# Kernel optimization log

Measured on AMD Instinct MI355X. Metric: run time of the kernel, lower is better.

The kernel has to match this reference:

```python
import jax, jax.numpy as jnp
import numpy as np
from jax import lax

B, T, P, H, O = 64, 96, 256, 128, 24  # batch, seq_len, num_points, hidden_dim, pred_len


def setup_inputs() -> dict:
    key = jax.random.key(0)
    ks = jax.random.split(key, 7)
    s = 1.0 / np.sqrt(H)  # torch LSTM/Linear default init scale
    return {
        "x": jax.random.normal(ks[0], (B, T, P, 1), dtype=jnp.float32),
        "W_ih": jax.random.uniform(ks[1], (P, 4 * H, 1), jnp.float32, -s, s),
        "W_hh": jax.random.uniform(ks[2], (P, 4 * H, H), jnp.float32, -s, s),
        "b_ih": jax.random.uniform(ks[3], (P, 4 * H), jnp.float32, -s, s),
        "b_hh": jax.random.uniform(ks[4], (P, 4 * H), jnp.float32, -s, s),
        "W_fc": jax.random.uniform(ks[5], (P, O, H), jnp.float32, -s, s),
        "b_fc": jax.random.uniform(ks[6], (P, O), jnp.float32, -s, s),
    }


def reference(x, W_ih, W_hh, b_ih, b_hh, W_fc, b_fc):
    # x: [B, T, P, F]; model uses only feature 0
    xs = x[..., 0]  # [B, T, P]
    # input_dim == 1, so input-to-gate contribution is a scaled broadcast of W_ih
    # precompute for all timesteps: [T, B, P, 4H]
    gx = jnp.einsum("btp,pg->tbpg", xs, W_ih[:, :, 0]) + (b_ih + b_hh)

    def step(carry, gxt):
        h, c = carry  # [B, P, H] each
        gates = gxt + jnp.einsum("bph,pgh->bpg", h, W_hh)  # [B, P, 4H]
        i, f, g, o = jnp.split(gates, 4, axis=-1)  # torch gate order i,f,g,o
        i = jax.nn.sigmoid(i)
        f = jax.nn.sigmoid(f)
        g = jnp.tanh(g)
        o = jax.nn.sigmoid(o)
        c = f * c + i * g
        h = o * jnp.tanh(c)
        return (h, c), None

    h0 = jnp.zeros((B, P, H), dtype=x.dtype)
    (h, _), _ = lax.scan(step, (h0, h0), gx)
    # per-point Linear on final hidden state: [B, P, O]
    out = jnp.einsum("bph,poh->bpo", h, W_fc) + b_fc
    # original stacks point outputs on last dim -> [B, pred_len, P]
    return jnp.transpose(out, (0, 2, 1))
```

## Files before the change

kernel.cpp:

```cpp
#include <hip/hip_runtime.h>
#include <hip/hip_bf16.h>

#define Bdim 64
#define Tdim 96
#define Pdim 256
#define Hdim 128
#define Gdim 512
#define Odim 24
#define BH   32
#define WROW 132

typedef _Float16 f16x8 __attribute__((ext_vector_type(8)));
typedef float    f32x16 __attribute__((ext_vector_type(16)));

union H8 { uint2 u2[2]; unsigned short s[8]; _Float16 h[8]; f16x8 v; };
union HS { _Float16 h; unsigned short s; };

__device__ __forceinline__ float exp2_fast(float x) {
#if __has_builtin(__builtin_amdgcn_exp2f)
    return __builtin_amdgcn_exp2f(x);
#else
    return __expf(x * 0.6931471805599453f);
#endif
}

__global__ __launch_bounds__(1024, 4)
void lstm_fused(const float* __restrict__ x,
                const float* __restrict__ W_ih,
                const float* __restrict__ W_hh,
                const float* __restrict__ b_ih,
                const float* __restrict__ b_hh,
                const float* __restrict__ W_fc,
                const float* __restrict__ b_fc,
                float* __restrict__ out)
{
    __shared__ unsigned short hs[2][2][BH * WROW];

    const int p   = blockIdx.x;
    const int tid = threadIdx.x;
    const int w   = tid >> 6;
    const int l31 = tid & 31;
    const int hi  = (tid >> 5) & 1;

    const float L1 = 1.4426950408889634f;
    const float L2 = 2.0f * L1;

    for (int i = tid; i < 2 * 2 * BH * WROW; i += 1024) ((unsigned short*)hs)[i] = 0;

    f16x8 afr[9];
    {
        const int rp   = w * 32 + l31;
        const int orow = ((rp & 3) << 7) | (rp >> 2);
        const float sc = ((rp & 3) == 2) ? L2 : L1;
        const float* rowp = W_hh + (size_t)p * Gdim * Hdim + (size_t)orow * Hdim;
        #pragma unroll
        for (int ks = 0; ks < 8; ++ks) {
            int k0 = ks * 16 + hi * 8;
            float4 va = *(const float4*)(rowp + k0);
            float4 vb = *(const float4*)(rowp + k0 + 4);
            H8 u;
            u.h[0] = (_Float16)(sc * va.x); u.h[1] = (_Float16)(sc * va.y);
            u.h[2] = (_Float16)(sc * va.z); u.h[3] = (_Float16)(sc * va.w);
            u.h[4] = (_Float16)(sc * vb.x); u.h[5] = (_Float16)(sc * vb.y);
            u.h[6] = (_Float16)(sc * vb.z); u.h[7] = (_Float16)(sc * vb.w);
            afr[ks] = u.v;
        }
        H8 u9;
        #pragma unroll
        for (int j = 0; j < 8; ++j) u9.s[j] = 0;
        if (hi == 0) {
            u9.h[0] = (_Float16)(sc * W_ih[(size_t)p * Gdim + orow]);
            u9.h[1] = (_Float16)(sc * (b_ih[(size_t)p * Gdim + orow] +
                                       b_hh[(size_t)p * Gdim + orow]));
        }
        afr[8] = u9.v;
    }

    auto do_gemm = [&](const unsigned short* hb, float xv) -> f32x16 {
        f32x16 a;
        #pragma unroll
        for (int j = 0; j < 16; ++j) a[j] = 0.f;
        const char* hbase = (const char*)hb;
        #pragma unroll
        for (int ks = 0; ks < 8; ++ks) {
            int boff = l31 * (WROW * 2) + ks * 32 + hi * 16;
            H8 bb;
            bb.u2[0] = *(const uint2*)(hbase + boff);
            bb.u2[1] = *(const uint2*)(hbase + boff + 8);
            a = __builtin_amdgcn_mfma_f32_32x32x16_f16(afr[ks], bb.v, a, 0, 0, 0);
        }
        H8 bg;
        #pragma unroll
        for (int j = 0; j < 8; ++j) bg.s[j] = 0;
        if (hi == 0) { bg.h[0] = (_Float16)xv; bg.h[1] = (_Float16)1.0f; }
        a = __builtin_amdgcn_mfma_f32_32x32x16_f16(afr[8], bg.v, a, 0, 0, 0);
        return a;
    };

    auto do_ep = [&](const f32x16& a, float* cr, unsigned short* hw) {
        #pragma unroll
        for (int q = 0; q < 4; ++q) {
            float yi = a[4 * q + 0];
            float yf = a[4 * q + 1];
            float yg = a[4 * q + 2];
            float yo = a[4 * q + 3];
            float Ef = exp2_fast(-yf);
            float Ei = exp2_fast(-yi);
            float Eg = exp2_fast(yg);
            float t1 = 1.0f + Ef;
            float t2 = 1.0f + Ei;
            float t3 = Eg + 1.0f;
            float t4 = Eg - 1.0f;
            float den = (t1 * t2) * t3;
            float num = __builtin_fmaf(cr[q] * t2, t3, (L2 * t4) * t1);
            float cn  = num * __builtin_amdgcn_rcpf(den);
            cn = fminf(60.0f, fmaxf(-60.0f, cn));
            cr[q] = cn;
            float Eo = exp2_fast(-yo);
            float Ec = exp2_fast(cn);
            float hv = (Ec - 1.0f) * __builtin_amdgcn_rcpf((1.0f + Eo) * (Ec + 1.0f));
            HS s2; s2.h = (_Float16)hv;
            hw[l31 * WROW + (w * 8 + 2 * q + hi)] = s2.s;
        }
    };

    float cre0[4] = {0.f, 0.f, 0.f, 0.f};
    float cre1[4] = {0.f, 0.f, 0.f, 0.f};

    const float* xp0 = x + (size_t)((0 * BH + l31) * Tdim) * Pdim + p;
    const float* xp1 = x + (size_t)((1 * BH + l31) * Tdim) * Pdim + p;
    float xv0 = xp0[0];
    float xv1 = xp1[0];

    __syncthreads();

    int b0 = 0, b1 = 0;
    f32x16 acc0 = do_gemm(hs[0][b0], xv0);
    xv0 = xp0[(size_t)1 * Pdim];

    f32x16 acc1;
    for (int t = 0; t < Tdim; ++t) {
        acc1 = do_gemm(hs[1][b1], xv1);
        do_ep(acc0, cre0, hs[0][b0 ^ 1]);
        __syncthreads();
        b0 ^= 1;
        xv1 = (t + 1 < Tdim) ? xp1[(size_t)(t + 1) * Pdim] : 0.f;

        acc0 = do_gemm(hs[0][b0], xv0);
        do_ep(acc1, cre1, hs[1][b1 ^ 1]);
        __syncthreads();
        b1 ^= 1;
        xv0 = (t + 2 < Tdim) ? xp0[(size_t)(t + 2) * Pdim] : 0.f;
    }

    const float* wfc = W_fc + (size_t)p * Odim * Hdim;
    const float* bfc = b_fc + (size_t)p * Odim;
    for (int i = tid; i < Bdim * Odim; i += 1024) {
        int o = i % Odim;
        int b = i / Odim;
        const unsigned short* hr = (b < BH) ? (hs[0][b0] + b * WROW)
                                            : (hs[1][b1] + (b - BH) * WROW);
        float s = bfc[o];
        const float* wr = wfc + o * Hdim;
        #pragma unroll 8
        for (int k2 = 0; k2 < Hdim; ++k2) {
            HS s2; s2.s = hr[k2];
            s = __builtin_fmaf(wr[k2], (float)s2.h, s);
        }
        out[(size_t)b * Odim * Pdim + (size_t)o * Pdim + p] = s;
    }
}

extern "C" void kernel_launch(void* const* d_in, const int* in_sizes, int n_in,
                              void* d_out, int out_size, void* d_ws, size_t ws_size,
                              hipStream_t stream) {
    const float* x    = (const float*)d_in[0];
    const float* W_ih = (const float*)d_in[1];
    const float* W_hh = (const float*)d_in[2];
    const float* b_ih = (const float*)d_in[3];
    const float* b_hh = (const float*)d_in[4];
    const float* W_fc = (const float*)d_in[5];
    const float* b_fc = (const float*)d_in[6];
    float* out = (float*)d_out;

    lstm_fused<<<dim3(Pdim), dim3(1024), 0, stream>>>(x, W_ih, W_hh, b_ih, b_hh, W_fc, b_fc, out);
}
```

Measured before the change: 400.4 us.

## Merge batch-half pipeline into single step with one barrier and paired reciprocals

Replaces the staggered two-half schedule (GEMM of one half overlapped with epilogue of the other, two barriers per timestep) with a single step that runs both halves' MFMA chains interleaved, then a joint epilogue and one barrier. Reciprocals in the gate epilogue are shared between the two halves via a product trick, halving rcp count. This removes a barrier per timestep but gives up the cross-half overlap of matrix and transcendental work; the clamp on the cell value is tightened, which also limits overflow in the shared-reciprocal products.

```diff
diff --git a/kernel.cpp b/kernel.cpp
--- a/kernel.cpp
+++ b/kernel.cpp
@@ -12,6 +12,7 @@
 
 typedef _Float16 f16x8 __attribute__((ext_vector_type(8)));
 typedef float    f32x16 __attribute__((ext_vector_type(16)));
+typedef float    f32x2  __attribute__((ext_vector_type(2)));
 
 union H8 { uint2 u2[2]; unsigned short s[8]; _Float16 h[8]; f16x8 v; };
 union HS { _Float16 h; unsigned short s; };
@@ -76,81 +77,101 @@
         afr[8] = u9.v;
     }
 
-    auto do_gemm = [&](const unsigned short* hb, float xv) -> f32x16 {
-        f32x16 a;
-        #pragma unroll
-        for (int j = 0; j < 16; ++j) a[j] = 0.f;
-        const char* hbase = (const char*)hb;
-        #pragma unroll
-        for (int ks = 0; ks < 8; ++ks) {
-            int boff = l31 * (WROW * 2) + ks * 32 + hi * 16;
-            H8 bb;
-            bb.u2[0] = *(const uint2*)(hbase + boff);
-            bb.u2[1] = *(const uint2*)(hbase + boff + 8);
-            a = __builtin_amdgcn_mfma_f32_32x32x16_f16(afr[ks], bb.v, a, 0, 0, 0);
-        }
-        H8 bg;
-        #pragma unroll
-        for (int j = 0; j < 8; ++j) bg.s[j] = 0;
-        if (hi == 0) { bg.h[0] = (_Float16)xv; bg.h[1] = (_Float16)1.0f; }
-        a = __builtin_amdgcn_mfma_f32_32x32x16_f16(afr[8], bg.v, a, 0, 0, 0);
-        return a;
-    };
-
-    auto do_ep = [&](const f32x16& a, float* cr, unsigned short* hw) {
-        #pragma unroll
-        for (int q = 0; q < 4; ++q) {
-            float yi = a[4 * q + 0];
-            float yf = a[4 * q + 1];
-            float yg = a[4 * q + 2];
-            float yo = a[4 * q + 3];
-            float Ef = exp2_fast(-yf);
-            float Ei = exp2_fast(-yi);
-            float Eg = exp2_fast(yg);
-            float t1 = 1.0f + Ef;
-            float t2 = 1.0f + Ei;
-            float t3 = Eg + 1.0f;
-            float t4 = Eg - 1.0f;
-            float den = (t1 * t2) * t3;
-            float num = __builtin_fmaf(cr[q] * t2, t3, (L2 * t4) * t1);
-            float cn  = num * __builtin_amdgcn_rcpf(den);
-            cn = fminf(60.0f, fmaxf(-60.0f, cn));
-            cr[q] = cn;
-            float Eo = exp2_fast(-yo);
-            float Ec = exp2_fast(cn);
-            float hv = (Ec - 1.0f) * __builtin_amdgcn_rcpf((1.0f + Eo) * (Ec + 1.0f));
-            HS s2; s2.h = (_Float16)hv;
-            hw[l31 * WROW + (w * 8 + 2 * q + hi)] = s2.s;
-        }
-    };
-
-    float cre0[4] = {0.f, 0.f, 0.f, 0.f};
-    float cre1[4] = {0.f, 0.f, 0.f, 0.f};
+    f32x16 zacc;
+    #pragma unroll
+    for (int j = 0; j < 16; ++j) zacc[j] = 0.f;
+
+    f32x2 cre[4];
+    #pragma unroll
+    for (int q = 0; q < 4; ++q) cre[q] = f32x2{0.f, 0.f};
 
     const float* xp0 = x + (size_t)((0 * BH + l31) * Tdim) * Pdim + p;
     const float* xp1 = x + (size_t)((1 * BH + l31) * Tdim) * Pdim + p;
     float xv0 = xp0[0];
     float xv1 = xp1[0];
 
+    const int lbase = l31 * (WROW * 2);
+
     __syncthreads();
 
-    int b0 = 0, b1 = 0;
-    f32x16 acc0 = do_gemm(hs[0][b0], xv0);
-    xv0 = xp0[(size_t)1 * Pdim];
-
-    f32x16 acc1;
-    for (int t = 0; t < Tdim; ++t) {
-        acc1 = do_gemm(hs[1][b1], xv1);
-        do_ep(acc0, cre0, hs[0][b0 ^ 1]);
+    auto dostep = [&](const int cur, const int t) {
+        float xn0 = 0.f, xn1 = 0.f;
+        if (t + 1 < Tdim) {
+            xn0 = xp0[(size_t)(t + 1) * Pdim];
+            xn1 = xp1[(size_t)(t + 1) * Pdim];
+        }
+
+        const char* h0 = (const char*)hs[0][cur];
+        const char* h1 = (const char*)hs[1][cur];
+        f32x16 a0, a1;
+        #pragma unroll
+        for (int ks = 0; ks < 8; ++ks) {
+            int boff = lbase + ks * 32 + hi * 16;
+            H8 b0, b1;
+            b0.u2[0] = *(const uint2*)(h0 + boff);
+            b0.u2[1] = *(const uint2*)(h0 + boff + 8);
+            b1.u2[0] = *(const uint2*)(h1 + boff);
+            b1.u2[1] = *(const uint2*)(h1 + boff + 8);
+            a0 = __builtin_amdgcn_mfma_f32_32x32x16_f16(afr[ks], b0.v, ks ? a0 : zacc, 0, 0, 0);
+            a1 = __builtin_amdgcn_mfma_f32_32x32x16_f16(afr[ks], b1.v, ks ? a1 : zacc, 0, 0, 0);
+        }
+        {
+            H8 bg0, bg1;
+            #pragma unroll
+            for (int j = 0; j < 8; ++j) { bg0.s[j] = 0; bg1.s[j] = 0; }
+            if (hi == 0) {
+                bg0.h[0] = (_Float16)xv0; bg0.h[1] = (_Float16)1.0f;
+                bg1.h[0] = (_Float16)xv1; bg1.h[1] = (_Float16)1.0f;
+            }
+            a0 = __builtin_amdgcn_mfma_f32_32x32x16_f16(afr[8], bg0.v, a0, 0, 0, 0);
+            a1 = __builtin_amdgcn_mfma_f32_32x32x16_f16(afr[8], bg1.v, a1, 0, 0, 0);
+        }
+
+        unsigned short* w0 = hs[0][cur ^ 1];
+        unsigned short* w1 = hs[1][cur ^ 1];
+        #pragma unroll
+        for (int q = 0; q < 4; ++q) {
+            f32x2 yi = {a0[4 * q + 0], a1[4 * q + 0]};
+            f32x2 yf = {a0[4 * q + 1], a1[4 * q + 1]};
+            f32x2 yg = {a0[4 * q + 2], a1[4 * q + 2]};
+            f32x2 yo = {a0[4 * q + 3], a1[4 * q + 3]};
+            f32x2 Ef = {exp2_fast(-yf.x), exp2_fast(-yf.y)};
+            f32x2 Ei = {exp2_fast(-yi.x), exp2_fast(-yi.y)};
+            f32x2 Eg = {exp2_fast(yg.x),  exp2_fast(yg.y)};
+            f32x2 t1 = Ef + 1.0f;
+            f32x2 t2 = Ei + 1.0f;
+            f32x2 t3 = Eg + 1.0f;
+            f32x2 t4 = Eg - 1.0f;
+            f32x2 den = (t1 * t2) * t3;
+            f32x2 num = (cre[q] * t2) * t3 + (L2 * t4) * t1;
+            float D = den.x * den.y;
+            float r = __builtin_amdgcn_rcpf(D);
+            f32x2 inv = {r * den.y, r * den.x};
+            f32x2 cn  = num * inv;
+            cn.x = fminf(30.0f, fmaxf(-30.0f, cn.x));
+            cn.y = fminf(30.0f, fmaxf(-30.0f, cn.y));
+            cre[q] = cn;
+            f32x2 Eo = {exp2_fast(-yo.x), exp2_fast(-yo.y)};
+            f32x2 Ec = {exp2_fast(cn.x),  exp2_fast(cn.y)};
+            f32x2 d2 = (Eo + 1.0f) * (Ec + 1.0f);
+            float D2 = d2.x * d2.y;
+            float r2 = __builtin_amdgcn_rcpf(D2);
+            f32x2 j2 = {r2 * d2.y, r2 * d2.x};
+            f32x2 hv = (Ec - 1.0f) * j2;
+            HS ha; ha.h = (_Float16)hv.x;
+            HS hb; hb.h = (_Float16)hv.y;
+            int idx = l31 * WROW + (w * 8 + 2 * q + hi);
+            w0[idx] = ha.s;
+            w1[idx] = hb.s;
+        }
+
         __syncthreads();
-        b0 ^= 1;
-        xv1 = (t + 1 < Tdim) ? xp1[(size_t)(t + 1) * Pdim] : 0.f;
-
-        acc0 = do_gemm(hs[0][b0], xv0);
-        do_ep(acc1, cre1, hs[1][b1 ^ 1]);
-        __syncthreads();
-        b1 ^= 1;
-        xv0 = (t + 2 < Tdim) ? xp0[(size_t)(t + 2) * Pdim] : 0.f;
+        xv0 = xn0; xv1 = xn1;
+    };
+
+    for (int t = 0; t < Tdim; t += 2) {
+        dostep(0, t);
+        dostep(1, t + 1);
     }
 
     const float* wfc = W_fc + (size_t)p * Odim * Hdim;
@@ -158,8 +179,8 @@
     for (int i = tid; i < Bdim * Odim; i += 1024) {
         int o = i % Odim;
         int b = i / Odim;
-        const unsigned short* hr = (b < BH) ? (hs[0][b0] + b * WROW)
-                                            : (hs[1][b1] + (b - BH) * WROW);
+        const unsigned short* hr = (b < BH) ? (hs[0][0] + b * WROW)
+                                            : (hs[1][0] + (b - BH) * WROW);
         float s = bfc[o];
         const float* wr = wfc + o * Hdim;
         #pragma unroll 8
```

Measured after the change: 408.5 us. 2.0% more time.
